# Kernel optimization log

Measured on AMD Instinct MI355X. Metric: run time of the kernel, lower is better.

## Reference

```python
import jax, jax.numpy as jnp
import numpy as np

NH, NL, NP, GA = 8, 4, 4, 8  # num_heads, num_levels, num_points, grid_align_num
SHAPES = np.array([[128, 128], [64, 64], [32, 32], [16, 16]], dtype=np.int64)  # (W, H) per level


def _grid_sample(img, grid):
    """F.grid_sample bilinear, padding_mode='zeros', align_corners=False.
    img: [N,C,H,W], grid: [N,Hg,Wg,2] in [-1,1] (x,y). Returns [N,C,Hg,Wg]."""
    N, C, H, W = img.shape
    x = (grid[..., 0] + 1.0) * (W * 0.5) - 0.5
    y = (grid[..., 1] + 1.0) * (H * 0.5) - 0.5
    x0 = jnp.floor(x)
    y0 = jnp.floor(y)
    wx = (x - x0)[:, None]  # [N,1,Hg,Wg]
    wy = (y - y0)[:, None]
    x0i = x0.astype(jnp.int32)
    y0i = y0.astype(jnp.int32)
    img_flat = img.reshape(N, C, H * W)
    Hg, Wg = grid.shape[1], grid.shape[2]

    def tap(ix, iy):
        valid = (ix >= 0) & (ix < W) & (iy >= 0) & (iy < H)
        lin = jnp.clip(iy, 0, H - 1) * W + jnp.clip(ix, 0, W - 1)
        v = jnp.take_along_axis(img_flat, lin.reshape(N, 1, Hg * Wg), axis=2)
        return v.reshape(N, C, Hg, Wg) * valid[:, None].astype(img.dtype)

    v00 = tap(x0i, y0i)
    v01 = tap(x0i + 1, y0i)
    v10 = tap(x0i, y0i + 1)
    v11 = tap(x0i + 1, y0i + 1)
    return (v00 * (1 - wx) * (1 - wy) + v01 * wx * (1 - wy)
            + v10 * (1 - wx) * wy + v11 * wx * wy)


def setup_inputs() -> dict:
    key = jax.random.key(0)
    ks = jax.random.split(key, 6)
    bs, nq, E = 2, 16384, 256
    total = int((SHAPES[:, 0] * SHAPES[:, 1]).sum())  # 21760
    query = jax.random.normal(ks[0], (bs, nq, E), jnp.float32)
    value = jax.random.normal(ks[1], (bs, total, NH, E // NH), jnp.float32)
    reference_points = jax.random.uniform(ks[2], (bs, nq, 1, NL * 2), jnp.float32)
    W_off = jax.random.normal(ks[3], (NH * NL * NP * 2, E), jnp.float32) * 0.01
    # structured offset bias per init_weights (directional rays, radius ~ point index)
    thetas = jnp.arange(NH, dtype=jnp.float32) * (2.0 * np.pi / NH)
    gi = jnp.stack([jnp.cos(thetas), jnp.sin(thetas)], -1)  # [NH,2]
    gi = gi / jnp.max(jnp.abs(gi), axis=-1, keepdims=True)
    gi = jnp.tile(gi[:, None, None, :], (1, NL, NP, 1))
    gi = gi * jnp.arange(1, NP + 1, dtype=jnp.float32)[None, None, :, None]
    b_off = gi.reshape(-1)
    W_attn = jax.random.normal(ks[4], (NH * NL * NP, E), jnp.float32) * 0.01
    b_attn = jax.random.normal(ks[5], (NH * NL * NP,), jnp.float32) * 0.01
    return {"query": query, "value": value, "reference_points": reference_points,
            "W_off": W_off, "b_off": b_off, "W_attn": W_attn, "b_attn": b_attn,
            "spatial_shapes": np.asarray(SHAPES)}


def reference(query, value, reference_points, W_off, b_off, W_attn, b_attn, spatial_shapes):
    bs, nq, E = query.shape
    d = E // NH
    shapes = np.asarray(spatial_shapes)  # static [L,2] (W,H)

    # sampling offsets and locations (non-deploy path)
    off = (query @ W_off.T + b_off).reshape(bs, nq, NH, NL * NP * 2)
    ref = jnp.tile(reference_points, (1, 1, NH, NP)).reshape(bs, nq, NH, NL * NP * 2)
    # offset_normalizer: (1/spatial_shapes).repeat(1, NP).flatten() -> layout (l, p, xy)
    norm = jnp.asarray(np.tile(1.0 / shapes.astype(np.float32), (1, NP)).reshape(-1))
    loc = (ref + off * norm) * 2.0 - 1.0  # [bs, nq, NH, NL*NP*2]

    # attention weights: softmax over levels*points, regrouped to (L, G, P) layout
    attn = jax.nn.softmax((query @ W_attn.T + b_attn).reshape(bs, nq, NH, NL * NP), axis=-1)
    attn = (attn.reshape(bs, nq // GA, GA, NH, NL, NP)
            .transpose(0, 3, 1, 4, 2, 5)
            .reshape(bs * NH, 1, nq // GA, NL * GA * NP))

    grids = loc.reshape(bs, nq, NH, NL, NP, 2)
    outs = []
    start = 0
    for lvl in range(NL):
        W_, H_ = int(shapes[lvl, 0]), int(shapes[lvl, 1])
        n = H_ * W_
        v = value[:, start:start + n].transpose(0, 2, 3, 1).reshape(bs * NH, d, H_, W_)
        start += n
        g = grids[:, :, :, lvl].transpose(0, 2, 1, 3, 4).reshape(bs * NH, nq // GA, GA * NP, 2)
        outs.append(_grid_sample(v, g))  # [bs*NH, d, nq//GA, GA*NP]
    samp = jnp.concatenate(outs, axis=-1) * attn  # [bs*NH, d, nq//GA, NL*GA*NP]
    # reduce_sum linear with fixed 0/1 weight == sum over levels and points per group slot
    out = samp.reshape(bs * NH, d, nq // GA, NL, GA, NP).sum(axis=(3, 5))
    return out.reshape(bs, NH * d, nq)
```

## Files before the change

### kernel.cpp

```cpp
#include <hip/hip_runtime.h>
#include <hip/hip_bf16.h>


typedef __attribute__((ext_vector_type(4))) float    float4v;
typedef __attribute__((ext_vector_type(8))) _Float16 half8;
typedef __attribute__((ext_vector_type(4))) _Float16 half4;
typedef __attribute__((ext_vector_type(2))) _Float16 half2v;

#define NQ    16384
#define NTOK  21760
#define LREC  48

#define GEMM_BLOCKS 768
#define CONV_BLOCKS 5440

union H8 { half8 v; half2v p[4]; };

#define LDSTR 88
__global__ __launch_bounds__(256) void gemm_kernel(
    const float* __restrict__ qf,
    const float* __restrict__ Woff, const float* __restrict__ Wattn,
    const float* __restrict__ boff, const float* __restrict__ battn,
    _Float16* __restrict__ lh) {
  const int tid = threadIdx.x;

  __shared__ _Float16 As[128 * LDSTR];
  __shared__ _Float16 Bs[128 * LDSTR];

  const int lane = tid & 63;
  const int wv   = tid >> 6;
  const int wm   = wv >> 1, wn = wv & 1;
  const int quad = lane >> 4;
  const int r    = lane & 15;
  const int blockM = (blockIdx.x & 255) * 128;
  const int n0     = (blockIdx.x >> 8) * 128;

  float4v acc[4][4];
#pragma unroll
  for (int i = 0; i < 4; ++i)
#pragma unroll
    for (int j = 0; j < 4; ++j) acc[i][j] = (float4v){0.f, 0.f, 0.f, 0.f};

  for (int kc = 0; kc < 4; ++kc) {
    const int k0 = kc * 64;
    if (kc) __syncthreads();
#pragma unroll
    for (int it = 0; it < 8; ++it) {
      int idx = it * 256 + tid;
      int row = idx >> 4, k4 = idx & 15;
      float4v v = *(const float4v*)(qf + (size_t)(blockM + row) * 256 + k0 + k4 * 4);
      half4 o;
      o[0] = (_Float16)v[0]; o[1] = (_Float16)v[1];
      o[2] = (_Float16)v[2]; o[3] = (_Float16)v[3];
      *(half4*)&As[row * LDSTR + k4 * 4] = o;
    }
#pragma unroll
    for (int it = 0; it < 8; ++it) {
      int idx = it * 256 + tid;
      int row = idx >> 4, k4 = idx & 15;
      int n = n0 + row;
      const float* src = (n < 256) ? (Woff + (size_t)n * 256)
                                   : (Wattn + (size_t)(n - 256) * 256);
      float4v v = *(const float4v*)(src + k0 + k4 * 4);
      half4 o;
      o[0] = (_Float16)v[0]; o[1] = (_Float16)v[1];
      o[2] = (_Float16)v[2]; o[3] = (_Float16)v[3];
      *(half4*)&Bs[row * LDSTR + k4 * 4] = o;
    }
    __syncthreads();

#pragma unroll
    for (int kf = 0; kf < 2; ++kf) {
      const int ko = kf * 32 + quad * 8;
      half8 af[4], bf[4];
#pragma unroll
      for (int mi = 0; mi < 4; ++mi)
        af[mi] = *(const half8*)&As[(wm * 64 + mi * 16 + r) * LDSTR + ko];
#pragma unroll
      for (int ni = 0; ni < 4; ++ni)
        bf[ni] = *(const half8*)&Bs[(wn * 64 + ni * 16 + r) * LDSTR + ko];
#pragma unroll
      for (int mi = 0; mi < 4; ++mi)
#pragma unroll
        for (int ni = 0; ni < 4; ++ni)
          acc[mi][ni] = __builtin_amdgcn_mfma_f32_16x16x32_f16(af[mi], bf[ni], acc[mi][ni], 0, 0, 0);
    }
  }

#pragma unroll
  for (int mi = 0; mi < 4; ++mi) {
    const int mb = blockM + wm * 64 + mi * 16 + quad * 4;
#pragma unroll
    for (int ni = 0; ni < 4; ++ni) {
      const int n = n0 + wn * 64 + ni * 16 + r;
      const float bias = (n < 256) ? boff[n] : battn[n - 256];
      const int h    = (n < 256) ? (n >> 5) : ((n - 256) >> 4);
      const int slot = (n < 256) ? (n & 31) : (32 + ((n - 256) & 15));
#pragma unroll
      for (int reg = 0; reg < 4; ++reg) {
        const int bq = mb + reg;
        const int b = bq >> 14, q = bq & 16383;
        lh[((size_t)(b * 8 + h) * NQ + q) * LREC + slot] =
            (_Float16)(acc[mi][ni][reg] + bias);
      }
    }
  }
}

__global__ __launch_bounds__(256) void conv_kernel(
    const float* __restrict__ val, _Float16* __restrict__ vh) {
  const int bid   = blockIdx.x;
  const int xcd   = bid & 7;
  const int local = bid >> 3;
  const int sl    = (local >= 340) ? 1 : 0;
  const int hb    = xcd * 2 + sl;
  const int tokT  = local - sl * 340;
  const int tid   = threadIdx.x;
  const int c8    = tid & 3;
  const int tok   = tokT * 64 + (tid >> 2);
  const int b     = hb >> 3, h = hb & 7;

  const float* src = val + ((size_t)b * NTOK + tok) * 256 + h * 32 + c8 * 8;
  float4v v0 = *(const float4v*)src;
  float4v v1 = *(const float4v*)(src + 4);
  half8 o;
  o[0] = (_Float16)v0[0]; o[1] = (_Float16)v0[1];
  o[2] = (_Float16)v0[2]; o[3] = (_Float16)v0[3];
  o[4] = (_Float16)v1[0]; o[5] = (_Float16)v1[1];
  o[6] = (_Float16)v1[2]; o[7] = (_Float16)v1[3];
  *(half8*)(vh + ((size_t)hb * NTOK + tok) * 32 + c8 * 8) = o;
}

__global__ __launch_bounds__(256) void sample_kernel(
    const _Float16* __restrict__ vh, const float* __restrict__ refp,
    const _Float16* __restrict__ lh, float* __restrict__ out) {
  const int bid   = blockIdx.x;
  const int xcd   = bid & 7;
  const int local = bid >> 3;
  const int hb    = xcd * 2 + (local >> 10);
  const int qt    = local & 1023;
  const int h     = hb & 7;
  const int b     = hb >> 3;
  const int tid = threadIdx.x;

  __shared__ _Float16 wsm[16][16];
  {
    const int q16  = tid >> 4;
    const int slot = tid & 15;
    const float lg = (float)lh[((size_t)hb * NQ + qt * 16 + q16) * LREC + 32 + slot];
    float m = lg;
    m = fmaxf(m, __shfl_xor(m, 1));
    m = fmaxf(m, __shfl_xor(m, 2));
    m = fmaxf(m, __shfl_xor(m, 4));
    m = fmaxf(m, __shfl_xor(m, 8));
    const float e = __expf(lg - m);
    float s = e;
    s += __shfl_xor(s, 1);
    s += __shfl_xor(s, 2);
    s += __shfl_xor(s, 4);
    s += __shfl_xor(s, 8);
    wsm[q16][slot] = (_Float16)(e * (1.0f / s));
  }
  __syncthreads();

  const int c4 = tid & 3;
  const int l  = (tid >> 2) & 3;
  const int qi = tid >> 4;
  const int q  = qt * 16 + qi;
  const size_t bq = (size_t)b * NQ + q;
  const _Float16* rec = lh + ((size_t)hb * NQ + q) * LREC;

  const half8 oh = *(const half8*)(rec + l * 8);
  const half4 ownw = *(const half4*)&wsm[qi][l * 4];

  float4v rp0 = *(const float4v*)(refp + bq * 8);
  float4v rp1 = *(const float4v*)(refp + bq * 8 + 4);
  const float rpx[4] = {rp0[0], rp0[2], rp1[0], rp1[2]};
  const float rpy[4] = {rp0[1], rp0[3], rp1[1], rp1[3]};

  const int   W    = 128 >> l;
  const float fW   = (float)W;
  const int   base = (l == 0) ? 0 : (l == 1) ? 16384 : (l == 2) ? 20480 : 21504;
  const _Float16* vlev = vh + ((size_t)hb * NTOK + base) * 32 + c4 * 8;

  half2v accl0 = (half2v){(_Float16)0, (_Float16)0};
  half2v accl1 = (half2v){(_Float16)0, (_Float16)0};
  half2v accl2 = (half2v){(_Float16)0, (_Float16)0};
  half2v accl3 = (half2v){(_Float16)0, (_Float16)0};

#pragma unroll
  for (int p = 0; p < 4; ++p) {
    const float a  = (float)ownw[p];
    const float ox = (float)oh[p * 2];
    const float oy = (float)oh[p * 2 + 1];
    const float x = rpx[p] * fW + ox - 0.5f;
    const float y = rpy[p] * fW + oy - 0.5f;
    const float xf = floorf(x), yf = floorf(y);
    const float fx = x - xf, fy = y - yf;
    const int ix = (int)xf, iy = (int)yf;
    const int ix0 = min(max(ix, 0), W - 1);
    const int ix1 = min(max(ix + 1, 0), W - 1);
    const int iy0 = min(max(iy, 0), W - 1);
    const int iy1 = min(max(iy + 1, 0), W - 1);
    const float wx0 = ((unsigned)ix       < (unsigned)W) ? 1.f - fx : 0.f;
    const float wx1 = ((unsigned)(ix + 1) < (unsigned)W) ? fx       : 0.f;
    const float wy0 = ((unsigned)iy       < (unsigned)W) ? 1.f - fy : 0.f;
    const float wy1 = ((unsigned)(iy + 1) < (unsigned)W) ? fy       : 0.f;
    const _Float16 w00 = (_Float16)(a * wx0 * wy0);
    const _Float16 w01 = (_Float16)(a * wx1 * wy0);
    const _Float16 w10 = (_Float16)(a * wx0 * wy1);
    const _Float16 w11 = (_Float16)(a * wx1 * wy1);
    const half2v h00 = (half2v){w00, w00};
    const half2v h01 = (half2v){w01, w01};
    const half2v h10 = (half2v){w10, w10};
    const half2v h11 = (half2v){w11, w11};
    const _Float16* r0 = vlev + (size_t)(iy0 * W) * 32;
    const _Float16* r1 = vlev + (size_t)(iy1 * W) * 32;
    H8 t00, t01, t10, t11;
    t00.v = *(const half8*)(r0 + ix0 * 32);
    t01.v = *(const half8*)(r0 + ix1 * 32);
    t10.v = *(const half8*)(r1 + ix0 * 32);
    t11.v = *(const half8*)(r1 + ix1 * 32);
    accl0 += h00 * t00.p[0] + h01 * t01.p[0] + h10 * t10.p[0] + h11 * t11.p[0];
    accl1 += h00 * t00.p[1] + h01 * t01.p[1] + h10 * t10.p[1] + h11 * t11.p[1];
    accl2 += h00 * t00.p[2] + h01 * t01.p[2] + h10 * t10.p[2] + h11 * t11.p[2];
    accl3 += h00 * t00.p[3] + h01 * t01.p[3] + h10 * t10.p[3] + h11 * t11.p[3];
  }

  float acc0[4], acc1[4];
  acc0[0] = (float)accl0[0]; acc0[1] = (float)accl0[1];
  acc0[2] = (float)accl1[0]; acc0[3] = (float)accl1[1];
  acc1[0] = (float)accl2[0]; acc1[1] = (float)accl2[1];
  acc1[2] = (float)accl3[0]; acc1[3] = (float)accl3[1];

  __shared__ float sm[4][16][33];
#pragma unroll
  for (int j = 0; j < 4; ++j) {
    sm[l][qi][c4 * 8 + j]     = acc0[j];
    sm[l][qi][c4 * 8 + 4 + j] = acc1[j];
  }
  __syncthreads();
  const size_t obase = ((size_t)b * 256 + h * 32) * NQ + qt * 16;
#pragma unroll
  for (int i = 0; i < 2; ++i) {
    const int idx = i * 256 + tid;
    const int c  = idx >> 4;
    const int ql = idx & 15;
    const float v = ((sm[0][ql][c] + sm[1][ql][c]) + sm[2][ql][c]) + sm[3][ql][c];
    out[obase + (size_t)c * NQ + ql] = v;
  }
}

extern "C" void kernel_launch(void* const* d_in, const int* in_sizes, int n_in,
                              void* d_out, int out_size, void* d_ws, size_t ws_size,
                              hipStream_t stream) {
  const float* query = (const float*)d_in[0];
  const float* value = (const float*)d_in[1];
  const float* refp  = (const float*)d_in[2];
  const float* Woff  = (const float*)d_in[3];
  const float* boff  = (const float*)d_in[4];
  const float* Wattn = (const float*)d_in[5];
  const float* battn = (const float*)d_in[6];
  float* out = (float*)d_out;

  char* ws = (char*)d_ws;
  _Float16* vh = (_Float16*)ws;
  _Float16* lh = (_Float16*)(ws + 22282240);

  gemm_kernel<<<GEMM_BLOCKS, 256, 0, stream>>>(
      query, Woff, Wattn, boff, battn, lh);
  conv_kernel<<<CONV_BLOCKS, 256, 0, stream>>>(value, vh);
  sample_kernel<<<16384, 256, 0, stream>>>(vh, refp, lh, out);
}
```

Baseline: 203.0 us.

## Store value map with horizontally paired texels for two-load bilinear taps

The conversion kernel now writes each token's 32 half channels twice, once at its own position and once into the previous token's second half. Each 64-element record therefore holds texel x and x+1 side by side, with zero padding at the slice ends. The sampler can then fetch a horizontal pair with one base address and no per-tap x clamping. This trades doubled conversion writes and workspace for simpler sampling address math and better locality. A workspace-size check falls back to the old path when the buffer is too small.

Measured after the change: 202.8 us. About the same (-0.1%).

```diff
diff --git a/kernel.cpp b/kernel.cpp
--- a/kernel.cpp
+++ b/kernel.cpp
@@ -13,6 +13,7 @@
 
 #define GEMM_BLOCKS 768
 #define CONV_BLOCKS 5440
+#define SLICE_H 1392704
 
 union H8 { half8 v; half2v p[4]; };
 
@@ -104,6 +105,164 @@
             (_Float16)(acc[mi][ni][reg] + bias);
       }
     }
+  }
+}
+
+__global__ __launch_bounds__(256) void conv_pair_kernel(
+    const float* __restrict__ val, _Float16* __restrict__ vh) {
+  const int bid   = blockIdx.x;
+  const int xcd   = bid & 7;
+  const int local = bid >> 3;
+  const int sl    = (local >= 340) ? 1 : 0;
+  const int hb    = xcd * 2 + sl;
+  const int tokT  = local - sl * 340;
+  const int tid   = threadIdx.x;
+  const int c8    = tid & 3;
+  const int tok   = tokT * 64 + (tid >> 2);
+  const int b     = hb >> 3, h = hb & 7;
+
+  const float* src = val + ((size_t)b * NTOK + tok) * 256 + h * 32 + c8 * 8;
+  float4v v0 = *(const float4v*)src;
+  float4v v1 = *(const float4v*)(src + 4);
+  half8 o;
+  o[0] = (_Float16)v0[0]; o[1] = (_Float16)v0[1];
+  o[2] = (_Float16)v0[2]; o[3] = (_Float16)v0[3];
+  o[4] = (_Float16)v1[0]; o[5] = (_Float16)v1[1];
+  o[6] = (_Float16)v1[2]; o[7] = (_Float16)v1[3];
+
+  _Float16* sd = vh + (size_t)hb * SLICE_H + 64;
+  *(half8*)(sd + (size_t)tok * 64 + c8 * 8)      = o;
+  *(half8*)(sd + (size_t)tok * 64 - 32 + c8 * 8) = o;
+  if (tok == 0) {
+    half8 z;
+#pragma unroll
+    for (int k = 0; k < 8; ++k) z[k] = (_Float16)0;
+    *(half8*)(sd - 64 + c8 * 8) = z;
+  }
+  if (tok == NTOK - 1) {
+    half8 z;
+#pragma unroll
+    for (int k = 0; k < 8; ++k) z[k] = (_Float16)0;
+    *(half8*)(sd + (size_t)NTOK * 64 - 32 + c8 * 8) = z;
+  }
+}
+
+__global__ __launch_bounds__(256) void sample_pair_kernel(
+    const _Float16* __restrict__ vh, const float* __restrict__ refp,
+    const _Float16* __restrict__ lh, float* __restrict__ out) {
+  const int bid   = blockIdx.x;
+  const int xcd   = bid & 7;
+  const int local = bid >> 3;
+  const int hb    = xcd * 2 + (local >> 10);
+  const int qt    = local & 1023;
+  const int h     = hb & 7;
+  const int b     = hb >> 3;
+  const int tid = threadIdx.x;
+
+  __shared__ _Float16 wsm[16][16];
+  {
+    const int q16  = tid >> 4;
+    const int slot = tid & 15;
+    const float lg = (float)lh[((size_t)hb * NQ + qt * 16 + q16) * LREC + 32 + slot];
+    float m = lg;
+    m = fmaxf(m, __shfl_xor(m, 1));
+    m = fmaxf(m, __shfl_xor(m, 2));
+    m = fmaxf(m, __shfl_xor(m, 4));
+    m = fmaxf(m, __shfl_xor(m, 8));
+    const float e = __expf(lg - m);
+    float s = e;
+    s += __shfl_xor(s, 1);
+    s += __shfl_xor(s, 2);
+    s += __shfl_xor(s, 4);
+    s += __shfl_xor(s, 8);
+    wsm[q16][slot] = (_Float16)(e * (1.0f / s));
+  }
+  __syncthreads();
+
+  const int c4 = tid & 3;
+  const int l  = (tid >> 2) & 3;
+  const int qi = tid >> 4;
+  const int q  = qt * 16 + qi;
+  const size_t bq = (size_t)b * NQ + q;
+  const _Float16* rec = lh + ((size_t)hb * NQ + q) * LREC;
+
+  const half8 oh = *(const half8*)(rec + l * 8);
+  const half4 ownw = *(const half4*)&wsm[qi][l * 4];
+
+  float4v rp0 = *(const float4v*)(refp + bq * 8);
+  float4v rp1 = *(const float4v*)(refp + bq * 8 + 4);
+  const float rpx[4] = {rp0[0], rp0[2], rp1[0], rp1[2]};
+  const float rpy[4] = {rp0[1], rp0[3], rp1[1], rp1[3]};
+
+  const int   W    = 128 >> l;
+  const float fW   = (float)W;
+  const int   base = (l == 0) ? 0 : (l == 1) ? 16384 : (l == 2) ? 20480 : 21504;
+  const _Float16* vlev = vh + (size_t)hb * SLICE_H + 64 + (size_t)base * 64 + c4 * 8;
+
+  half2v accl0 = (half2v){(_Float16)0, (_Float16)0};
+  half2v accl1 = (half2v){(_Float16)0, (_Float16)0};
+  half2v accl2 = (half2v){(_Float16)0, (_Float16)0};
+  half2v accl3 = (half2v){(_Float16)0, (_Float16)0};
+
+#pragma unroll
+  for (int p = 0; p < 4; ++p) {
+    const float a  = (float)ownw[p];
+    const float ox = (float)oh[p * 2];
+    const float oy = (float)oh[p * 2 + 1];
+    const float x = rpx[p] * fW + ox - 0.5f;
+    const float y = rpy[p] * fW + oy - 0.5f;
+    const float xf = floorf(x), yf = floorf(y);
+    const float fx = x - xf, fy = y - yf;
+    const int ix = (int)xf, iy = (int)yf;
+    const int ax  = min(max(ix, -1), W - 1);
+    const int iy0 = min(max(iy, 0), W - 1);
+    const int iy1 = min(max(iy + 1, 0), W - 1);
+    const float wx0 = ((unsigned)ix       < (unsigned)W) ? 1.f - fx : 0.f;
+    const float wx1 = ((unsigned)(ix + 1) < (unsigned)W) ? fx       : 0.f;
+    const float wy0 = ((unsigned)iy       < (unsigned)W) ? 1.f - fy : 0.f;
+    const float wy1 = ((unsigned)(iy + 1) < (unsigned)W) ? fy       : 0.f;
+    const _Float16 w00 = (_Float16)(a * wx0 * wy0);
+    const _Float16 w01 = (_Float16)(a * wx1 * wy0);
+    const _Float16 w10 = (_Float16)(a * wx0 * wy1);
+    const _Float16 w11 = (_Float16)(a * wx1 * wy1);
+    const half2v h00 = (half2v){w00, w00};
+    const half2v h01 = (half2v){w01, w01};
+    const half2v h10 = (half2v){w10, w10};
+    const half2v h11 = (half2v){w11, w11};
+    const _Float16* e0 = vlev + (iy0 * W + ax) * 64;
+    const _Float16* e1 = vlev + (iy1 * W + ax) * 64;
+    H8 t00, t01, t10, t11;
+    t00.v = *(const half8*)(e0);
+    t01.v = *(const half8*)(e0 + 32);
+    t10.v = *(const half8*)(e1);
+    t11.v = *(const half8*)(e1 + 32);
+    accl0 += h00 * t00.p[0] + h01 * t01.p[0] + h10 * t10.p[0] + h11 * t11.p[0];
+    accl1 += h00 * t00.p[1] + h01 * t01.p[1] + h10 * t10.p[1] + h11 * t11.p[1];
+    accl2 += h00 * t00.p[2] + h01 * t01.p[2] + h10 * t10.p[2] + h11 * t11.p[2];
+    accl3 += h00 * t00.p[3] + h01 * t01.p[3] + h10 * t10.p[3] + h11 * t11.p[3];
+  }
+
+  float acc0[4], acc1[4];
+  acc0[0] = (float)accl0[0]; acc0[1] = (float)accl0[1];
+  acc0[2] = (float)accl1[0]; acc0[3] = (float)accl1[1];
+  acc1[0] = (float)accl2[0]; acc1[1] = (float)accl2[1];
+  acc1[2] = (float)accl3[0]; acc1[3] = (float)accl3[1];
+
+  __shared__ float sm[4][16][33];
+#pragma unroll
+  for (int j = 0; j < 4; ++j) {
+    sm[l][qi][c4 * 8 + j]     = acc0[j];
+    sm[l][qi][c4 * 8 + 4 + j] = acc1[j];
+  }
+  __syncthreads();
+  const size_t obase = ((size_t)b * 256 + h * 32) * NQ + qt * 16;
+#pragma unroll
+  for (int i = 0; i < 2; ++i) {
+    const int idx = i * 256 + tid;
+    const int c  = idx >> 4;
+    const int ql = idx & 15;
+    const float v = ((sm[0][ql][c] + sm[1][ql][c]) + sm[2][ql][c]) + sm[3][ql][c];
+    out[obase + (size_t)c * NQ + ql] = v;
   }
 }
 
@@ -264,11 +423,22 @@
   float* out = (float*)d_out;
 
   char* ws = (char*)d_ws;
-  _Float16* vh = (_Float16*)ws;
-  _Float16* lh = (_Float16*)(ws + 22282240);
-
-  gemm_kernel<<<GEMM_BLOCKS, 256, 0, stream>>>(
-      query, Woff, Wattn, boff, battn, lh);
-  conv_kernel<<<CONV_BLOCKS, 256, 0, stream>>>(value, vh);
-  sample_kernel<<<16384, 256, 0, stream>>>(vh, refp, lh, out);
-}
+  const size_t PAIR_VH_BYTES = (size_t)16 * SLICE_H * 2;
+  const size_t LH_BYTES      = 25165824;
+
+  if (ws_size >= PAIR_VH_BYTES + LH_BYTES) {
+    _Float16* vh = (_Float16*)ws;
+    _Float16* lh = (_Float16*)(ws + PAIR_VH_BYTES);
+    gemm_kernel<<<GEMM_BLOCKS, 256, 0, stream>>>(
+        query, Woff, Wattn, boff, battn, lh);
+    conv_pair_kernel<<<CONV_BLOCKS, 256, 0, stream>>>(value, vh);
+    sample_pair_kernel<<<16384, 256, 0, stream>>>(vh, refp, lh, out);
+  } else {
+    _Float16* vh = (_Float16*)ws;
+    _Float16* lh = (_Float16*)(ws + 22282240);
+    gemm_kernel<<<GEMM_BLOCKS, 256, 0, stream>>>(
+        query, Woff, Wattn, boff, battn, lh);
+    conv_kernel<<<CONV_BLOCKS, 256, 0, stream>>>(value, vh);
+    sample_kernel<<<16384, 256, 0, stream>>>(vh, refp, lh, out);
+  }
+}
```
